# Kernel optimization log

Measured on AMD Instinct MI355X. Metric: run time of the kernel, lower is better.

The kernel has to match this reference:

```python
import jax, jax.numpy as jnp
import numpy as np

D_MODEL = 1440; D_INNER = 2880; D_STATE = 128; HEADDIM = 64; NHEADS = 45
D_CONV = 4; NLAYERS = 32; VOCAB = 256; CHUNK = 128
D_XBC = D_INNER + 2 * D_STATE          # 3136 conv channels
D_PROJ = 2 * D_INNER + 2 * D_STATE + NHEADS  # 6061 in_proj width
EPS = 1e-5

def silu(x):
    return x * jax.nn.sigmoid(x)

def segsum(x):
    # x: (..., T) -> (..., T, T); out[i, j] = sum_{j < k <= i} x[k], -inf above diagonal
    T = x.shape[-1]
    xe = jnp.broadcast_to(x[..., None], (*x.shape, T))
    lower = jnp.tril(jnp.ones((T, T), bool), -1)
    cs = jnp.cumsum(jnp.where(lower, xe, 0.0), axis=-2)
    return jnp.where(jnp.tril(jnp.ones((T, T), bool)), cs, -jnp.inf)

def ssd(X, A, B, C):
    # Chunked SSD (Mamba2 'ssd_minimal_discrete'). X:(b,l,h,p) pre-multiplied by dt,
    # A:(b,l,h) = dt * A_head, B/C:(b,l,n) (ngroups=1, shared across heads).
    b, l, h, p = X.shape
    n = B.shape[-1]
    c = l // CHUNK
    Xc = X.reshape(b, c, CHUNK, h, p)
    Ac = A.reshape(b, c, CHUNK, h).transpose(0, 3, 1, 2)      # (b,h,c,q)
    Bc = B.reshape(b, c, CHUNK, n)
    Cc = C.reshape(b, c, CHUNK, n)
    A_cs = jnp.cumsum(Ac, axis=-1)                            # (b,h,c,q)
    L = jnp.exp(segsum(Ac))                                   # (b,h,c,q,q) intra-chunk decay
    Y_diag = jnp.einsum('bcln,bcsn,bhcls,bcshp->bclhp', Cc, Bc, L, Xc)
    decay_states = jnp.exp(A_cs[..., -1:] - A_cs)             # (b,h,c,q)
    states = jnp.einsum('bcln,bhcl,bclhp->bchpn', Bc, decay_states, Xc)
    A_last = jnp.pad(A_cs[..., -1], ((0, 0), (0, 0), (1, 0)))  # (b,h,c+1)
    decay_chunk = jnp.exp(segsum(A_last))                     # (b,h,c+1,c+1)
    states = jnp.concatenate([jnp.zeros_like(states[:, :1]), states], axis=1)
    states = jnp.einsum('bhzc,bchpn->bzhpn', decay_chunk, states)[:, :-1]  # (b,c,h,p,n)
    Y_off = jnp.einsum('bcln,bchpn,bhcl->bclhp', Cc, states, jnp.exp(A_cs))
    return (Y_diag + Y_off).reshape(b, l, h, p)

def mamba2_block(h, p):
    Win, conv_w, conv_b, dt_bias, A_log, Dp, norm_w, Wout = p
    b, l, _ = h.shape
    zxbcdt = h @ Win                                           # (b,l,6061)
    z = zxbcdt[..., :D_INNER]
    xBC = zxbcdt[..., D_INNER:D_INNER + D_XBC]
    dt = jax.nn.softplus(zxbcdt[..., -NHEADS:] + dt_bias)      # (b,l,H)
    # causal depthwise conv over time, kernel 4
    xp = jnp.pad(xBC, ((0, 0), (D_CONV - 1, 0), (0, 0))).transpose(0, 2, 1)  # (b,C,l+3)
    xBC = jax.lax.conv_general_dilated(xp, conv_w[:, None, :], (1,), 'VALID',
            feature_group_count=D_XBC, dimension_numbers=('NCH', 'OIH', 'NCH'))
    xBC = silu(xBC.transpose(0, 2, 1) + conv_b)                # (b,l,3136)
    x = xBC[..., :D_INNER].reshape(b, l, NHEADS, HEADDIM)
    B = xBC[..., D_INNER:D_INNER + D_STATE]
    C = xBC[..., D_INNER + D_STATE:]
    A = -jnp.exp(A_log)                                        # (H,)
    y = ssd(x * dt[..., None], dt * A, B, C)
    y = y + x * Dp[None, None, :, None]                        # D skip (on raw x)
    y = y.reshape(b, l, D_INNER) * silu(z)                     # gate, then RMSNormGated
    y = y * jax.lax.rsqrt(jnp.mean(y * y, -1, keepdims=True) + EPS) * norm_w
    return y @ Wout

def setup_inputs() -> dict:
    key = jax.random.key(0)
    ks = jax.random.split(key, 8)
    b, l = 2, 2048
    def nrm(k, shape, s=0.02):
        return jax.random.normal(k, shape, jnp.float32) * s
    tokens = jax.random.randint(ks[0], (b, l), 0, VOCAB)
    embed = nrm(ks[1], (VOCAB, D_MODEL))
    Win = nrm(ks[2], (NLAYERS, D_MODEL, D_PROJ))
    conv_w = nrm(ks[3], (NLAYERS, D_XBC, D_CONV), 0.2)
    conv_b = jnp.zeros((NLAYERS, D_XBC), jnp.float32)
    dtv = jnp.exp(jax.random.uniform(ks[4], (NLAYERS, NHEADS)) * (np.log(0.1) - np.log(1e-3)) + np.log(1e-3))
    dt_bias = dtv + jnp.log(-jnp.expm1(-dtv))                  # inverse softplus
    A_log = jnp.log(jax.random.uniform(ks[5], (NLAYERS, NHEADS), minval=1.0, maxval=16.0))
    Dp = jnp.ones((NLAYERS, NHEADS), jnp.float32)
    norm_w = jnp.ones((NLAYERS, D_INNER), jnp.float32)
    Wout = nrm(ks[6], (NLAYERS, D_INNER, D_MODEL))
    final_norm_w = jnp.ones((D_MODEL,), jnp.float32)
    return {'tokens': tokens, 'embed': embed, 'Win': Win, 'conv_w': conv_w,
            'conv_b': conv_b, 'dt_bias': dt_bias, 'A_log': A_log, 'Dp': Dp,
            'norm_w': norm_w, 'Wout': Wout, 'final_norm_w': final_norm_w}

def reference(tokens, embed, Win, conv_w, conv_b, dt_bias, A_log, Dp, norm_w, Wout, final_norm_w):
    h = embed[tokens]                                          # (b,l,d)
    layer_params = (Win, conv_w, conv_b, dt_bias, A_log, Dp, norm_w, Wout)
    def step(carry, p):
        return carry + mamba2_block(carry, p), None
    h, _ = jax.lax.scan(jax.checkpoint(step), h, layer_params)
    h = h * jax.lax.rsqrt(jnp.mean(h * h, -1, keepdims=True) + EPS) * final_norm_w
    return h @ embed.T                                         # tied head -> (b,l,256)
```

## Files before the change

### kernel.cpp

```cpp
#include <hip/hip_runtime.h>
#include <hip/hip_bf16.h>
#include <math.h>

#define NLAYERS 32
#define DM 1440
#define DI 2880
#define DSTATE 128
#define HD 64
#define NH 45
#define VOCABSZ 256
#define CHUNK 128
#define DXBC 3136
#define DPROJ 6061
#define BB 2
#define LL 2048
#define ROWS (BB*LL)
#define NCH (LL/CHUNK)
#define ZXS 6144
#define STR 136
#define STR2 68

typedef __attribute__((ext_vector_type(8))) short bf16x8;
typedef __attribute__((ext_vector_type(4))) float f32x4;
typedef unsigned short us;

__device__ __forceinline__ float sigmoidf_(float x){ return 1.0f/(1.0f+__expf(-x)); }
__device__ __forceinline__ us f2b(float f){
  unsigned int u = __float_as_uint(f);
  return (us)((u + 0x7FFFu + ((u>>16)&1u)) >> 16);
}
__device__ __forceinline__ float b2f(us s){
  return __uint_as_float(((unsigned int)s)<<16);
}
__device__ __forceinline__ void split2(float v, us* ph, us* pl){
  us h = f2b(v);
  *ph = h;
  *pl = f2b(v - b2f(h));
}
__device__ __forceinline__ void gl2lds16(const us* g, us* l){
  __builtin_amdgcn_global_load_lds((const __attribute__((address_space(1))) unsigned int*)g,
                                   (__attribute__((address_space(3))) unsigned int*)l, 16, 0, 0);
}
#define MFMA(a,b,c) __builtin_amdgcn_mfma_f32_16x16x32_bf16(a,b,c,0,0,0)

__global__ void k_embed(const int* __restrict__ tok, const float* __restrict__ emb, float* __restrict__ h){
  int idx = blockIdx.x*256 + threadIdx.x;
  if (idx >= ROWS*DM) return;
  int row = idx / DM, d = idx - row*DM;
  h[idx] = emb[tok[row]*DM + d];
}

__global__ void k_split_rows(const float* __restrict__ src, us* __restrict__ dh,
                             us* __restrict__ dl, int ncols){
  size_t e = ((size_t)blockIdx.x*256 + threadIdx.x)*8;
  const float* s = src + e;
  bf16x8 oh, ol;
  #pragma unroll
  for (int j=0;j<8;j++){
    float v = s[j];
    us hh = f2b(v);
    ((us*)&oh)[j] = hh;
    ((us*)&ol)[j] = f2b(v - b2f(hh));
  }
  *(bf16x8*)(dh + e) = oh;
  *(bf16x8*)(dl + e) = ol;
}

__global__ void k_transcast_sp(const float* __restrict__ W, us* __restrict__ WTh,
                               us* __restrict__ WTl, int K, int N){
  __shared__ float t[32][65];
  int tid = threadIdx.x;
  int n0 = blockIdx.x*64, k0 = blockIdx.y*32;
  #pragma unroll
  for (int i=0;i<8;i++){
    int e = i*256 + tid;
    int r = e >> 6, cc = e & 63;
    int n = n0 + cc;
    t[r][cc] = (n < N) ? W[(size_t)(k0+r)*N + n] : 0.f;
  }
  __syncthreads();
  int nrow = tid >> 2, kseg = (tid & 3)*8;
  bf16x8 oh, ol;
  #pragma unroll
  for (int j=0;j<8;j++){
    float v = t[kseg+j][nrow];
    us hh = f2b(v);
    ((us*)&oh)[j] = hh;
    ((us*)&ol)[j] = f2b(v - b2f(hh));
  }
  *(bf16x8*)(WTh + (size_t)(n0+nrow)*K + k0 + kseg) = oh;
  *(bf16x8*)(WTl + (size_t)(n0+nrow)*K + k0 + kseg) = ol;
}

template<bool ACC, bool SPL>
__global__ __launch_bounds__(256) void k_gemm_sp(const us* __restrict__ Ah, const us* __restrict__ Al,
      const us* __restrict__ Bh, const us* __restrict__ Bl, float* __restrict__ C,
      int K, int ldc, int N, int nbx, us* __restrict__ Oh, us* __restrict__ Ol){
  __shared__ __align__(16) us sAh[4096], sAl[4096], sBh[4096], sBl[4096];
  int nwg = gridDim.x;
  int q = nwg >> 3;
  int bid = blockIdx.x;
  int wg = (bid & 7)*q + (bid >> 3);
  int grp = wg / (4*nbx);
  int rem = wg - grp*4*nbx;
  int by = grp*4 + (rem & 3);
  int bx = rem >> 2;
  int m0 = by*128, n0 = bx*128;
  int tid = threadIdx.x;
  int lane = tid & 63, wid = tid >> 6;
  int wr = wid >> 1, wc = wid & 1;
  int r4 = lane >> 2, c4 = (lane & 3)*8;
  int fr = lane & 15, fk = (lane >> 4)*8;
  f32x4 acc[4][4];
  #pragma unroll
  for (int i=0;i<4;i++)
    #pragma unroll
    for (int j=0;j<4;j++) acc[i][j] = (f32x4){0.f,0.f,0.f,0.f};
  for (int kt = 0; kt < K; kt += 32){
    __syncthreads();
    size_t ra0 = (size_t)(m0 + wid*16     + r4)*K + kt + c4;
    size_t ra1 = (size_t)(m0 + (wid+4)*16 + r4)*K + kt + c4;
    size_t rb0 = (size_t)(n0 + wid*16     + r4)*K + kt + c4;
    size_t rb1 = (size_t)(n0 + (wid+4)*16 + r4)*K + kt + c4;
    gl2lds16(Ah + ra0, sAh + wid*512);
    gl2lds16(Ah + ra1, sAh + (wid+4)*512);
    gl2lds16(Al + ra0, sAl + wid*512);
    gl2lds16(Al + ra1, sAl + (wid+4)*512);
    gl2lds16(Bh + rb0, sBh + wid*512);
    gl2lds16(Bh + rb1, sBh + (wid+4)*512);
    gl2lds16(Bl + rb0, sBl + wid*512);
    gl2lds16(Bl + rb1, sBl + (wid+4)*512);
    __syncthreads();
    bf16x8 ah[4], al[4], bh[4], bl[4];
    #pragma unroll
    for (int i=0;i<4;i++){
      int ro = (wr*64 + i*16 + fr)*32 + fk;
      int co = (wc*64 + i*16 + fr)*32 + fk;
      ah[i] = *(const bf16x8*)(sAh + ro);
      al[i] = *(const bf16x8*)(sAl + ro);
      bh[i] = *(const bf16x8*)(sBh + co);
      bl[i] = *(const bf16x8*)(sBl + co);
    }
    #pragma unroll
    for (int i=0;i<4;i++)
      #pragma unroll
      for (int j=0;j<4;j++){
        acc[i][j] = MFMA(ah[i], bh[j], acc[i][j]);
        acc[i][j] = MFMA(ah[i], bl[j], acc[i][j]);
        acc[i][j] = MFMA(al[i], bh[j], acc[i][j]);
      }
  }
  int orow = (lane>>4)*4, ocol = lane & 15;
  #pragma unroll
  for (int i=0;i<4;i++)
    #pragma unroll
    for (int j=0;j<4;j++)
      #pragma unroll
      for (int r=0;r<4;r++){
        int col = n0 + wc*64 + j*16 + ocol;
        if (col < N){
          size_t off = (size_t)(m0 + wr*64 + i*16 + orow + r)*ldc + col;
          float v = acc[i][j][r] + (ACC ? C[off] : 0.f);
          C[off] = v;
          if (SPL) split2(v, &Oh[off], &Ol[off]);
        }
      }
}

__global__ __launch_bounds__(256) void k_conv2(const float* __restrict__ zx, const float* __restrict__ cw,
                        const float* __restrict__ cb, us* __restrict__ xbh, us* __restrict__ xbl,
                        const float* __restrict__ dtb_in, float* __restrict__ dtb){
  int ch = blockIdx.x*256 + threadIdx.x;
  int l0 = blockIdx.y * 16;
  int b = blockIdx.z;
  if (ch < DXBC){
    float w0 = cw[ch*4+0], w1 = cw[ch*4+1], w2 = cw[ch*4+2], w3 = cw[ch*4+3];
    float bias = cb[ch];
    float x0=0.f, x1=0.f, x2=0.f;
    if (l0-3 >= 0) x0 = zx[(size_t)(b*LL + l0-3)*ZXS + DI + ch];
    if (l0-2 >= 0) x1 = zx[(size_t)(b*LL + l0-2)*ZXS + DI + ch];
    if (l0-1 >= 0) x2 = zx[(size_t)(b*LL + l0-1)*ZXS + DI + ch];
    #pragma unroll 4
    for (int l = l0; l < l0+16; ++l){
      float x3 = zx[(size_t)(b*LL + l)*ZXS + DI + ch];
      float s = bias + w0*x0 + w1*x1 + w2*x2 + w3*x3;
      float v = s * sigmoidf_(s);
      size_t off = (size_t)(b*LL + l)*DXBC + ch;
      split2(v, &xbh[off], &xbl[off]);
      x0 = x1; x1 = x2; x2 = x3;
    }
  } else if (ch < DXBC + NH){
    int hh = ch - DXBC;
    float bias = dtb_in[hh];
    #pragma unroll 4
    for (int l = l0; l < l0+16; ++l){
      size_t row = (size_t)(b*LL + l);
      float v = zx[row*ZXS + (DI+DXBC) + hh] + bias;
      dtb[row*NH + hh] = (v > 20.f) ? v : log1pf(__expf(v));
    }
  }
}

__global__ __launch_bounds__(256) void k_sraw(const us* __restrict__ xbh, const us* __restrict__ xbl,
                                              float* __restrict__ Sraw){
  __shared__ __align__(16) us sCh[128*STR], sCl[128*STR], sB2h[128*STR], sB2l[128*STR];
  int tid = threadIdx.x;
  int c = blockIdx.x, b = blockIdx.y;
  int t0 = b*LL + c*CHUNK;
  #pragma unroll
  for (int i=0;i<8;i++){
    int e = i*256 + tid;
    int l = e >> 4, seg = (e & 15)*8;
    size_t oc = (size_t)(t0+l)*DXBC + DI + DSTATE + seg;
    size_t ob = (size_t)(t0+l)*DXBC + DI + seg;
    *(bf16x8*)(sCh + l*STR + seg) = *(const bf16x8*)(xbh + oc);
    *(bf16x8*)(sCl + l*STR + seg) = *(const bf16x8*)(xbl + oc);
    *(bf16x8*)(sB2h + l*STR + seg) = *(const bf16x8*)(xbh + ob);
    *(bf16x8*)(sB2l + l*STR + seg) = *(const bf16x8*)(xbl + ob);
  }
  __syncthreads();
  int lane = tid & 63, wid = tid >> 6;
  int wbase = wid*32;
  int fr = lane & 15, fk = (lane>>4)*8;
  int orow = (lane>>4)*4;
  f32x4 accS[2][8];
  #pragma unroll
  for (int m=0;m<2;m++)
    #pragma unroll
    for (int j=0;j<8;j++) accS[m][j] = (f32x4){0.f,0.f,0.f,0.f};
  #pragma unroll
  for (int ks=0; ks<4; ++ks){
    int ko = ks*32 + fk;
    bf16x8 a0h = *(const bf16x8*)(sCh + (wbase+fr)*STR + ko);
    bf16x8 a0l = *(const bf16x8*)(sCl + (wbase+fr)*STR + ko);
    bf16x8 a1h = *(const bf16x8*)(sCh + (wbase+16+fr)*STR + ko);
    bf16x8 a1l = *(const bf16x8*)(sCl + (wbase+16+fr)*STR + ko);
    #pragma unroll
    for (int j=0;j<8;j++){
      bf16x8 bh = *(const bf16x8*)(sB2h + (j*16+fr)*STR + ko);
      bf16x8 bl = *(const bf16x8*)(sB2l + (j*16+fr)*STR + ko);
      accS[0][j] = MFMA(a0h, bh, accS[0][j]);
      accS[0][j] = MFMA(a0h, bl, accS[0][j]);
      accS[0][j] = MFMA(a0l, bh, accS[0][j]);
      accS[1][j] = MFMA(a1h, bh, accS[1][j]);
      accS[1][j] = MFMA(a1h, bl, accS[1][j]);
      accS[1][j] = MFMA(a1l, bh, accS[1][j]);
    }
  }
  size_t sbase = ((size_t)(b*NCH + c))*16384;
  #pragma unroll
  for (int m=0;m<2;m++)
    #pragma unroll
    for (int j=0;j<8;j++)
      #pragma unroll
      for (int r=0;r<4;r++){
        int l = wbase + m*16 + orow + r;
        int s = j*16 + fr;
        Sraw[sbase + l*128 + s] = accS[m][j][r];
      }
}

__global__ __launch_bounds__(256) void k_ssd_state_sp(const us* __restrict__ xbh, const us* __restrict__ xbl,
    const float* __restrict__ dtb, const float* __restrict__ Alog,
    float* __restrict__ acs, us* __restrict__ cst_h, us* __restrict__ cst_l){
  __shared__ __align__(16) us sBTh[64*STR], sBTl[64*STR];
  __shared__ __align__(16) us sXTh[64*STR], sXTl[64*STR];
  __shared__ float sAcs[128];
  __shared__ float sDt[128];
  int tid = threadIdx.x;
  int hh = blockIdx.x, c = blockIdx.y, b = blockIdx.z;
  int t0 = b*LL + c*CHUNK;
  float A_h = -__expf(Alog[hh]);
  if (tid < 128){
    float d = dtb[(size_t)(t0+tid)*NH + hh];
    sDt[tid] = d;
    sAcs[tid] = d * A_h;
  }
  __syncthreads();
  if (tid < 64){
    float v = sAcs[tid], w = sAcs[64+tid];
    #pragma unroll
    for (int off=1; off<64; off<<=1){
      float tv = __shfl_up(v, off, 64);
      float tw = __shfl_up(w, off, 64);
      if (tid >= off){ v += tv; w += tw; }
    }
    float tot = __shfl(v, 63, 64);
    sAcs[tid] = v;
    sAcs[64+tid] = w + tot;
  }
  __syncthreads();
  if (tid < 128) acs[(size_t)(t0+tid)*NH + hh] = sAcs[tid];
  float alast = sAcs[127];
  #pragma unroll 8
  for (int i=0;i<32;i++){
    int e = i*256 + tid;
    int l = e >> 6, p = e & 63;
    size_t off = (size_t)(t0+l)*DXBC + hh*HD + p;
    float v = (b2f(xbh[off]) + b2f(xbl[off])) * sDt[l] * __expf(alast - sAcs[l]);
    split2(v, &sXTh[p*STR+l], &sXTl[p*STR+l]);
  }
  int lane = tid & 63, wid = tid >> 6;
  int fr = lane & 15, fk = (lane>>4)*8;
  f32x4 acc[8];
  #pragma unroll
  for (int j=0;j<8;j++) acc[j] = (f32x4){0.f,0.f,0.f,0.f};
  #pragma unroll
  for (int nh=0; nh<2; ++nh){
    __syncthreads();
    #pragma unroll 8
    for (int i=0;i<32;i++){
      int e = i*256 + tid;
      int l = e >> 6, n = e & 63;
      size_t off = (size_t)(t0+l)*DXBC + DI + nh*64 + n;
      sBTh[n*STR+l] = xbh[off];
      sBTl[n*STR+l] = xbl[off];
    }
    __syncthreads();
    #pragma unroll
    for (int ks=0; ks<4; ks++){
      bf16x8 ah = *(const bf16x8*)(sXTh + (wid*16 + fr)*STR + ks*32 + fk);
      bf16x8 al = *(const bf16x8*)(sXTl + (wid*16 + fr)*STR + ks*32 + fk);
      #pragma unroll
      for (int j=0;j<4;j++){
        bf16x8 bh = *(const bf16x8*)(sBTh + (j*16 + fr)*STR + ks*32 + fk);
        bf16x8 bl = *(const bf16x8*)(sBTl + (j*16 + fr)*STR + ks*32 + fk);
        acc[nh*4+j] = MFMA(ah, bh, acc[nh*4+j]);
        acc[nh*4+j] = MFMA(ah, bl, acc[nh*4+j]);
        acc[nh*4+j] = MFMA(al, bh, acc[nh*4+j]);
      }
    }
  }
  size_t cbase = (((size_t)(b*NCH + c)*NH) + hh)*8192;
  int orow = (lane>>4)*4;
  #pragma unroll
  for (int jj=0;jj<8;jj++)
    #pragma unroll
    for (int r=0;r<4;r++){
      int p = wid*16 + orow + r;
      int n = (jj>>2)*64 + (jj&3)*16 + fr;
      split2(acc[jj][r], &cst_h[cbase + p*128 + n], &cst_l[cbase + p*128 + n]);
    }
}

__global__ __launch_bounds__(256) void k_ssd_scan2(const float* __restrict__ acs,
      us* __restrict__ cst_h, us* __restrict__ cst_l){
  int tid = threadIdx.x;
  int hh = blockIdx.x, b = blockIdx.y, z = blockIdx.z;
  int base_e = z*1024;
  float P[4];
  #pragma unroll
  for (int i=0;i<4;i++) P[i] = 0.f;
  for (int c=0;c<NCH;c++){
    size_t base = (((size_t)(b*NCH + c)*NH) + hh)*8192 + base_e;
    float dec = __expf(acs[(size_t)(b*LL + c*CHUNK + CHUNK-1)*NH + hh]);
    #pragma unroll
    for (int i=0;i<4;i++){
      size_t e = base + i*256 + tid;
      float tmp = b2f(cst_h[e]) + b2f(cst_l[e]);
      split2(P[i], &cst_h[e], &cst_l[e]);
      P[i] = dec*P[i] + tmp;
    }
  }
}

__global__ __launch_bounds__(512) void k_ssd_y_sp(const us* __restrict__ xbh, const us* __restrict__ xbl,
    const float* __restrict__ dtb, const float* __restrict__ acs,
    const us* __restrict__ cst_h, const us* __restrict__ cst_l,
    const float* __restrict__ Sraw, float* __restrict__ Yf){
  __shared__ __align__(16) us sXh[64*STR], sXl[64*STR];
  __shared__ float sAcs[128];
  __shared__ float sDt[128];
  int tid = threadIdx.x;
  int hh = blockIdx.x, c = blockIdx.y, b = blockIdx.z;
  int t0 = b*LL + c*CHUNK;
  if (tid < 128){
    sAcs[tid] = acs[(size_t)(t0+tid)*NH + hh];
    sDt[tid]  = dtb[(size_t)(t0+tid)*NH + hh];
  }
  #pragma unroll 8
  for (int i=0;i<16;i++){
    int e = i*512 + tid;
    int s = e >> 6, p = e & 63;
    size_t off = (size_t)(t0+s)*DXBC + hh*HD + p;
    sXh[p*STR + s] = xbh[off];
    sXl[p*STR + s] = xbl[off];
  }
  __syncthreads();
  int lane = tid & 63, wid = tid >> 6;
  int wbase = wid*16;
  int fr = lane & 15, fk = (lane>>4)*8;
  int orow = (lane>>4)*4;
  int l = wbase + fr;
  float acs_l = sAcs[l];
  size_t cbase = (((size_t)(b*NCH + c)*NH) + hh)*8192;
  size_t sbase = ((size_t)(b*NCH + c))*16384;
  size_t crow  = (size_t)(t0+l)*DXBC + DI + DSTATE;

  f32x4 accU[4], accD[4];
  #pragma unroll
  for (int j=0;j<4;j++){
    accU[j] = (f32x4){0.f,0.f,0.f,0.f};
    accD[j] = (f32x4){0.f,0.f,0.f,0.f};
  }
  #pragma unroll
  for (int kk=0; kk<4; ++kk){
    int ko = kk*32 + fk;
    bf16x8 ch8 = *(const bf16x8*)(xbh + crow + ko);
    bf16x8 cl8 = *(const bf16x8*)(xbl + crow + ko);
    #pragma unroll
    for (int j=0;j<4;j++){
      int prow = j*16 + fr;
      bf16x8 ph = *(const bf16x8*)(cst_h + cbase + prow*128 + ko);
      bf16x8 pl = *(const bf16x8*)(cst_l + cbase + prow*128 + ko);
      accU[j] = MFMA(ch8, ph, accU[j]);
      accU[j] = MFMA(ch8, pl, accU[j]);
      accU[j] = MFMA(cl8, ph, accU[j]);
    }
  }
  #pragma unroll
  for (int kk=0; kk<4; ++kk){
    int sc = kk*32 + fk;
    const float* rp = Sraw + sbase + (size_t)l*128 + sc;
    bf16x8 ah, al;
    #pragma unroll
    for (int jj=0;jj<8;jj++){
      int s = sc + jj;
      float v = (s <= l) ? rp[jj]*__expf(acs_l - sAcs[s])*sDt[s] : 0.f;
      us h2 = f2b(v);
      ((us*)&ah)[jj] = h2;
      ((us*)&al)[jj] = f2b(v - b2f(h2));
    }
    #pragma unroll
    for (int j=0;j<4;j++){
      bf16x8 xh = *(const bf16x8*)(sXh + (j*16+fr)*STR + sc);
      bf16x8 xl = *(const bf16x8*)(sXl + (j*16+fr)*STR + sc);
      accD[j] = MFMA(ah, xh, accD[j]);
      accD[j] = MFMA(ah, xl, accD[j]);
      accD[j] = MFMA(al, xh, accD[j]);
    }
  }
  #pragma unroll
  for (int r=0;r<4;r++){
    int lo = wbase + orow + r;
    float ea = __expf(sAcs[lo]);
    #pragma unroll
    for (int j=0;j<4;j++)
      Yf[(size_t)(t0+lo)*DI + hh*HD + j*16 + fr] = accD[j][r] + ea*accU[j][r];
  }
}

__global__ __launch_bounds__(256) void k_gatenorm(const float* __restrict__ Yf,
                           const us* __restrict__ xbh, const us* __restrict__ xbl,
                           const float* __restrict__ zx, const float* __restrict__ Dp_l,
                           const float* __restrict__ nw, us* __restrict__ yh, us* __restrict__ yl){
  __shared__ float red[4];
  __shared__ float stot;
  int row = blockIdx.x;
  int tid = threadIdx.x;
  float yv_[12];
  float ss = 0.f;
  #pragma unroll
  for (int i=0;i<12;i++){
    int d = tid + i*256;
    if (d < DI){
      size_t xo = (size_t)row*DXBC + d;
      float xv = b2f(xbh[xo]) + b2f(xbl[xo]);
      float yv = Yf[(size_t)row*DI + d] + xv * Dp_l[d >> 6];
      float zv = zx[(size_t)row*ZXS + d];
      yv *= zv * sigmoidf_(zv);
      yv_[i] = yv;
      ss += yv*yv;
    } else yv_[i] = 0.f;
  }
  #pragma unroll
  for (int off=32; off>0; off>>=1) ss += __shfl_down(ss, off, 64);
  int lane = tid & 63, wid = tid >> 6;
  if (lane == 0) red[wid] = ss;
  __syncthreads();
  if (tid == 0) stot = red[0]+red[1]+red[2]+red[3];
  __syncthreads();
  float rs = rsqrtf(stot / (float)DI + 1e-5f);
  #pragma unroll
  for (int i=0;i<12;i++){
    int d = tid + i*256;
    if (d < DI){
      float v = yv_[i] * rs * nw[d];
      split2(v, &yh[(size_t)row*DI + d], &yl[(size_t)row*DI + d]);
    }
  }
}

__global__ __launch_bounds__(256) void k_finalnorm(const float* __restrict__ h, const float* __restrict__ fnw,
                            us* __restrict__ oh, us* __restrict__ ol){
  __shared__ float red[4];
  __shared__ float stot;
  int row = blockIdx.x;
  int tid = threadIdx.x;
  float v_[6];
  float ss = 0.f;
  #pragma unroll
  for (int i=0;i<6;i++){
    int d = tid + i*256;
    if (d < DM){ v_[i] = h[(size_t)row*DM + d]; ss += v_[i]*v_[i]; }
    else v_[i] = 0.f;
  }
  #pragma unroll
  for (int off=32; off>0; off>>=1) ss += __shfl_down(ss, off, 64);
  int lane = tid & 63, wid = tid >> 6;
  if (lane == 0) red[wid] = ss;
  __syncthreads();
  if (tid == 0) stot = red[0]+red[1]+red[2]+red[3];
  __syncthreads();
  float rs = rsqrtf(stot / (float)DM + 1e-5f);
  #pragma unroll
  for (int i=0;i<6;i++){
    int d = tid + i*256;
    if (d < DM){
      float v = v_[i] * rs * fnw[d];
      split2(v, &oh[(size_t)row*DM + d], &ol[(size_t)row*DM + d]);
    }
  }
}

extern "C" void kernel_launch(void* const* d_in, const int* in_sizes, int n_in,
                              void* d_out, int out_size, void* d_ws, size_t ws_size,
                              hipStream_t stream){
  const int*   tok   = (const int*)d_in[0];
  const float* emb   = (const float*)d_in[1];
  const float* Win   = (const float*)d_in[2];
  const float* convw = (const float*)d_in[3];
  const float* convb = (const float*)d_in[4];
  const float* dtbias= (const float*)d_in[5];
  const float* Alog  = (const float*)d_in[6];
  const float* Dp    = (const float*)d_in[7];
  const float* normw = (const float*)d_in[8];
  const float* Wout  = (const float*)d_in[9];
  const float* fnw   = (const float*)d_in[10];

  float* ws = (float*)d_ws;
  float* h    = ws;
  float* zx   = ws + 5898240;
  us*    xbh  = (us*)(ws + 31064064);
  us*    xbl  = (us*)(ws + 37486592);
  us*    hp_h = (us*)(ws + 31064064);
  us*    hp_l = (us*)(ws + 34013184);
  float* dtb  = ws + 43909120;
  float* acs  = ws + 44093440;
  float* Yf   = ws + 44277760;
  us* wbuf_h  = (us*)(ws + 44277760);
  us* wbuf_l  = (us*)(ws + 48701440);
  us* cst_h   = (us*)(ws + 56074240);
  us* cst_l   = (us*)(ws + 61972480);
  us* ab_h    = (us*)(ws + 56074240);
  us* ab_l    = (us*)(ws + 61972480);
  float* Sraw = ws + 67870720;

  k_embed<<<(ROWS*DM+255)/256, 256, 0, stream>>>(tok, emb, h);
  k_split_rows<<<2880, 256, 0, stream>>>(h, hp_h, hp_l, DM);
  for (int lyr=0; lyr<NLAYERS; ++lyr){
    k_transcast_sp<<<dim3(ZXS/64, DM/32), 256, 0, stream>>>(Win + (size_t)lyr*DM*DPROJ, wbuf_h, wbuf_l, DM, DPROJ);
    k_gemm_sp<false,false><<<(ZXS/128)*(ROWS/128), 256, 0, stream>>>(hp_h, hp_l, wbuf_h, wbuf_l, zx, DM, ZXS, ZXS, ZXS/128, nullptr, nullptr);
    k_conv2<<<dim3(13, 128, BB), 256, 0, stream>>>(
        zx, convw + (size_t)lyr*DXBC*4, convb + (size_t)lyr*DXBC, xbh, xbl,
        dtbias + lyr*NH, dtb);
    k_sraw<<<dim3(NCH, BB), 256, 0, stream>>>(xbh, xbl, Sraw);
    k_ssd_state_sp<<<dim3(NH, NCH, BB), 256, 0, stream>>>(xbh, xbl, dtb, Alog + lyr*NH, acs, cst_h, cst_l);
    k_ssd_scan2<<<dim3(NH, BB, 8), 256, 0, stream>>>(acs, cst_h, cst_l);
    k_ssd_y_sp<<<dim3(NH, NCH, BB), 512, 0, stream>>>(xbh, xbl, dtb, acs, cst_h, cst_l, Sraw, Yf);
    k_gatenorm<<<ROWS, 256, 0, stream>>>(Yf, xbh, xbl, zx, Dp + lyr*NH, normw + (size_t)lyr*DI, ab_h, ab_l);
    k_transcast_sp<<<dim3(1536/64, DI/32), 256, 0, stream>>>(Wout + (size_t)lyr*DI*DM, wbuf_h, wbuf_l, DI, DM);
    k_gemm_sp<true,true><<<(1536/128)*(ROWS/128), 256, 0, stream>>>(ab_h, ab_l, wbuf_h, wbuf_l, h, DI, DM, DM, 1536/128, hp_h, hp_l);
  }
  k_finalnorm<<<ROWS, 256, 0, stream>>>(h, fnw, ab_h, ab_l);
  k_split_rows<<<180, 256, 0, stream>>>(emb, wbuf_h, wbuf_l, DM);
  k_gemm_sp<false,false><<<(VOCABSZ/128)*(ROWS/128), 256, 0, stream>>>(ab_h, ab_l, wbuf_h, wbuf_l, (float*)d_out, DM, VOCABSZ, VOCABSZ, VOCABSZ/128, nullptr, nullptr);
}
```

Measured before the change: 19.63 ms.

## Precompute transposed B per chunk once in sraw; read it directly in state kernel

```diff
diff --git a/kernel.cpp b/kernel.cpp
--- a/kernel.cpp
+++ b/kernel.cpp
@@ -202,7 +202,8 @@
 }
 
 __global__ __launch_bounds__(256) void k_sraw(const us* __restrict__ xbh, const us* __restrict__ xbl,
-                                              float* __restrict__ Sraw){
+                                              float* __restrict__ Sraw,
+                                              us* __restrict__ BTh, us* __restrict__ BTl){
   __shared__ __align__(16) us sCh[128*STR], sCl[128*STR], sB2h[128*STR], sB2l[128*STR];
   int tid = threadIdx.x;
   int c = blockIdx.x, b = blockIdx.y;
@@ -219,6 +220,14 @@
     *(bf16x8*)(sB2l + l*STR + seg) = *(const bf16x8*)(xbl + ob);
   }
   __syncthreads();
+  size_t btb = ((size_t)(b*NCH + c))*16384;
+  #pragma unroll
+  for (int i=0;i<64;i++){
+    int e = i*256 + tid;
+    int n = e >> 7, l = e & 127;
+    BTh[btb + n*128 + l] = sB2h[l*STR + n];
+    BTl[btb + n*128 + l] = sB2l[l*STR + n];
+  }
   int lane = tid & 63, wid = tid >> 6;
   int wbase = wid*32;
   int fr = lane & 15, fk = (lane>>4)*8;
@@ -260,10 +269,10 @@
       }
 }
 
-__global__ __launch_bounds__(256) void k_ssd_state_sp(const us* __restrict__ xbh, const us* __restrict__ xbl,
+__global__ __launch_bounds__(512) void k_ssd_state_sp(const us* __restrict__ xbh, const us* __restrict__ xbl,
     const float* __restrict__ dtb, const float* __restrict__ Alog,
+    const us* __restrict__ BTh, const us* __restrict__ BTl,
     float* __restrict__ acs, us* __restrict__ cst_h, us* __restrict__ cst_l){
-  __shared__ __align__(16) us sBTh[64*STR], sBTl[64*STR];
   __shared__ __align__(16) us sXTh[64*STR], sXTl[64*STR];
   __shared__ float sAcs[128];
   __shared__ float sDt[128];
@@ -293,53 +302,46 @@
   if (tid < 128) acs[(size_t)(t0+tid)*NH + hh] = sAcs[tid];
   float alast = sAcs[127];
   #pragma unroll 8
-  for (int i=0;i<32;i++){
-    int e = i*256 + tid;
+  for (int i=0;i<16;i++){
+    int e = i*512 + tid;
     int l = e >> 6, p = e & 63;
     size_t off = (size_t)(t0+l)*DXBC + hh*HD + p;
     float v = (b2f(xbh[off]) + b2f(xbl[off])) * sDt[l] * __expf(alast - sAcs[l]);
     split2(v, &sXTh[p*STR+l], &sXTl[p*STR+l]);
   }
+  __syncthreads();
   int lane = tid & 63, wid = tid >> 6;
   int fr = lane & 15, fk = (lane>>4)*8;
-  f32x4 acc[8];
-  #pragma unroll
-  for (int j=0;j<8;j++) acc[j] = (f32x4){0.f,0.f,0.f,0.f};
-  #pragma unroll
-  for (int nh=0; nh<2; ++nh){
-    __syncthreads();
-    #pragma unroll 8
-    for (int i=0;i<32;i++){
-      int e = i*256 + tid;
-      int l = e >> 6, n = e & 63;
-      size_t off = (size_t)(t0+l)*DXBC + DI + nh*64 + n;
-      sBTh[n*STR+l] = xbh[off];
-      sBTl[n*STR+l] = xbl[off];
-    }
-    __syncthreads();
-    #pragma unroll
-    for (int ks=0; ks<4; ks++){
-      bf16x8 ah = *(const bf16x8*)(sXTh + (wid*16 + fr)*STR + ks*32 + fk);
-      bf16x8 al = *(const bf16x8*)(sXTl + (wid*16 + fr)*STR + ks*32 + fk);
-      #pragma unroll
-      for (int j=0;j<4;j++){
-        bf16x8 bh = *(const bf16x8*)(sBTh + (j*16 + fr)*STR + ks*32 + fk);
-        bf16x8 bl = *(const bf16x8*)(sBTl + (j*16 + fr)*STR + ks*32 + fk);
-        acc[nh*4+j] = MFMA(ah, bh, acc[nh*4+j]);
-        acc[nh*4+j] = MFMA(ah, bl, acc[nh*4+j]);
-        acc[nh*4+j] = MFMA(al, bh, acc[nh*4+j]);
-      }
+  int pr = (wid & 3)*16;
+  int nb = (wid >> 2)*64;
+  size_t btb = ((size_t)(b*NCH + c))*16384;
+  f32x4 acc[4];
+  #pragma unroll
+  for (int j=0;j<4;j++) acc[j] = (f32x4){0.f,0.f,0.f,0.f};
+  #pragma unroll
+  for (int ks=0; ks<4; ks++){
+    int ko = ks*32 + fk;
+    bf16x8 ah = *(const bf16x8*)(sXTh + (pr + fr)*STR + ko);
+    bf16x8 al = *(const bf16x8*)(sXTl + (pr + fr)*STR + ko);
+    #pragma unroll
+    for (int j=0;j<4;j++){
+      int nrow = nb + j*16 + fr;
+      bf16x8 bh = *(const bf16x8*)(BTh + btb + nrow*128 + ko);
+      bf16x8 bl = *(const bf16x8*)(BTl + btb + nrow*128 + ko);
+      acc[j] = MFMA(ah, bh, acc[j]);
+      acc[j] = MFMA(ah, bl, acc[j]);
+      acc[j] = MFMA(al, bh, acc[j]);
     }
   }
   size_t cbase = (((size_t)(b*NCH + c)*NH) + hh)*8192;
   int orow = (lane>>4)*4;
   #pragma unroll
-  for (int jj=0;jj<8;jj++)
+  for (int j=0;j<4;j++)
     #pragma unroll
     for (int r=0;r<4;r++){
-      int p = wid*16 + orow + r;
-      int n = (jj>>2)*64 + (jj&3)*16 + fr;
-      split2(acc[jj][r], &cst_h[cbase + p*128 + n], &cst_l[cbase + p*128 + n]);
+      int p = pr + orow + r;
+      int n = nb + j*16 + fr;
+      split2(acc[j][r], &cst_h[cbase + p*128 + n], &cst_l[cbase + p*128 + n]);
     }
 }
 
@@ -555,6 +557,8 @@
   us* ab_h    = (us*)(ws + 56074240);
   us* ab_l    = (us*)(ws + 61972480);
   float* Sraw = ws + 67870720;
+  us*    BTh  = (us*)(ws + 68395008);
+  us*    BTl  = (us*)(ws + 68657152);
 
   k_embed<<<(ROWS*DM+255)/256, 256, 0, stream>>>(tok, emb, h);
   k_split_rows<<<2880, 256, 0, stream>>>(h, hp_h, hp_l, DM);
@@ -564,8 +568,8 @@
     k_conv2<<<dim3(13, 128, BB), 256, 0, stream>>>(
         zx, convw + (size_t)lyr*DXBC*4, convb + (size_t)lyr*DXBC, xbh, xbl,
         dtbias + lyr*NH, dtb);
-    k_sraw<<<dim3(NCH, BB), 256, 0, stream>>>(xbh, xbl, Sraw);
-    k_ssd_state_sp<<<dim3(NH, NCH, BB), 256, 0, stream>>>(xbh, xbl, dtb, Alog + lyr*NH, acs, cst_h, cst_l);
+    k_sraw<<<dim3(NCH, BB), 256, 0, stream>>>(xbh, xbl, Sraw, BTh, BTl);
+    k_ssd_state_sp<<<dim3(NH, NCH, BB), 512, 0, stream>>>(xbh, xbl, dtb, Alog + lyr*NH, BTh, BTl, acs, cst_h, cst_l);
     k_ssd_scan2<<<dim3(NH, BB, 8), 256, 0, stream>>>(acs, cst_h, cst_l);
     k_ssd_y_sp<<<dim3(NH, NCH, BB), 512, 0, stream>>>(xbh, xbl, dtb, acs, cst_h, cst_l, Sraw, Yf);
     k_gatenorm<<<ROWS, 256, 0, stream>>>(Yf, xbh, xbl, zx, Dp + lyr*NH, normw + (size_t)lyr*DI, ab_h, ab_l);
```

Result: slower. 20.15 ms (+2.6%).

## Fuse weight transpose-casts into GEMM launches and swizzle LDS transpose stores

Applied to the files above, without the earlier changes.

```diff
diff --git a/kernel.cpp b/kernel.cpp
--- a/kernel.cpp
+++ b/kernel.cpp
@@ -18,7 +18,6 @@
 #define NCH (LL/CHUNK)
 #define ZXS 6144
 #define STR 136
-#define STR2 68
 
 typedef __attribute__((ext_vector_type(8))) short bf16x8;
 typedef __attribute__((ext_vector_type(4))) float f32x4;
@@ -95,18 +94,46 @@
 template<bool ACC, bool SPL>
 __global__ __launch_bounds__(256) void k_gemm_sp(const us* __restrict__ Ah, const us* __restrict__ Al,
       const us* __restrict__ Bh, const us* __restrict__ Bl, float* __restrict__ C,
-      int K, int ldc, int N, int nbx, us* __restrict__ Oh, us* __restrict__ Ol){
-  __shared__ __align__(16) us sAh[4096], sAl[4096], sBh[4096], sBl[4096];
-  int nwg = gridDim.x;
-  int q = nwg >> 3;
+      int K, int ldc, int N, int nbx, us* __restrict__ Oh, us* __restrict__ Ol,
+      int ngemm, const float* __restrict__ tcW, us* __restrict__ tcH, us* __restrict__ tcL,
+      int tcK, int tcN, int tcNBX){
+  __shared__ __align__(16) us smem[16384];
   int bid = blockIdx.x;
+  int tid = threadIdx.x;
+  if (bid >= ngemm){
+    int t = bid - ngemm;
+    int n0 = (t % tcNBX)*64, k0 = (t / tcNBX)*32;
+    float* tt = (float*)smem;
+    #pragma unroll
+    for (int i=0;i<8;i++){
+      int e = i*256 + tid;
+      int r = e >> 6, cc = e & 63;
+      int n = n0 + cc;
+      tt[r*65+cc] = (n < tcN) ? tcW[(size_t)(k0+r)*tcN + n] : 0.f;
+    }
+    __syncthreads();
+    int nrow = tid >> 2, kseg = (tid & 3)*8;
+    bf16x8 oh, ol;
+    #pragma unroll
+    for (int j=0;j<8;j++){
+      float v = tt[(kseg+j)*65 + nrow];
+      us hh = f2b(v);
+      ((us*)&oh)[j] = hh;
+      ((us*)&ol)[j] = f2b(v - b2f(hh));
+    }
+    *(bf16x8*)(tcH + (size_t)(n0+nrow)*tcK + k0 + kseg) = oh;
+    *(bf16x8*)(tcL + (size_t)(n0+nrow)*tcK + k0 + kseg) = ol;
+    return;
+  }
+  us* sAh = smem;        us* sAl = smem + 4096;
+  us* sBh = smem + 8192; us* sBl = smem + 12288;
+  int q = ngemm >> 3;
   int wg = (bid & 7)*q + (bid >> 3);
   int grp = wg / (4*nbx);
   int rem = wg - grp*4*nbx;
   int by = grp*4 + (rem & 3);
   int bx = rem >> 2;
   int m0 = by*128, n0 = bx*128;
-  int tid = threadIdx.x;
   int lane = tid & 63, wid = tid >> 6;
   int wr = wid >> 1, wc = wid & 1;
   int r4 = lane >> 2, c4 = (lane & 3)*8;
@@ -294,8 +321,9 @@
   float alast = sAcs[127];
   #pragma unroll 8
   for (int i=0;i<32;i++){
-    int e = i*256 + tid;
-    int l = e >> 6, p = e & 63;
+    int idx = i*256 + tid;
+    int j = idx & 7, g = (idx>>3) & 7, pm = (idx>>6) & 7, lm = idx>>9;
+    int p = pm*8 + j, l = lm*8 + g;
     size_t off = (size_t)(t0+l)*DXBC + hh*HD + p;
     float v = (b2f(xbh[off]) + b2f(xbl[off])) * sDt[l] * __expf(alast - sAcs[l]);
     split2(v, &sXTh[p*STR+l], &sXTl[p*STR+l]);
@@ -310,8 +338,9 @@
     __syncthreads();
     #pragma unroll 8
     for (int i=0;i<32;i++){
-      int e = i*256 + tid;
-      int l = e >> 6, n = e & 63;
+      int idx = i*256 + tid;
+      int j = idx & 7, g = (idx>>3) & 7, nm = (idx>>6) & 7, lm = idx>>9;
+      int n = nm*8 + j, l = lm*8 + g;
       size_t off = (size_t)(t0+l)*DXBC + DI + nh*64 + n;
       sBTh[n*STR+l] = xbh[off];
       sBTl[n*STR+l] = xbl[off];
@@ -380,8 +409,9 @@
   }
   #pragma unroll 8
   for (int i=0;i<16;i++){
-    int e = i*512 + tid;
-    int s = e >> 6, p = e & 63;
+    int idx = i*512 + tid;
+    int j = idx & 7, g = (idx>>3) & 7, pm = (idx>>6) & 7, lm = idx>>9;
+    int p = pm*8 + j, s = lm*8 + g;
     size_t off = (size_t)(t0+s)*DXBC + hh*HD + p;
     sXh[p*STR + s] = xbh[off];
     sXl[p*STR + s] = xbl[off];
@@ -548,19 +578,23 @@
   float* dtb  = ws + 43909120;
   float* acs  = ws + 44093440;
   float* Yf   = ws + 44277760;
-  us* wbuf_h  = (us*)(ws + 44277760);
-  us* wbuf_l  = (us*)(ws + 48701440);
   us* cst_h   = (us*)(ws + 56074240);
   us* cst_l   = (us*)(ws + 61972480);
   us* ab_h    = (us*)(ws + 56074240);
   us* ab_l    = (us*)(ws + 61972480);
   float* Sraw = ws + 67870720;
+  us* winh    = (us*)(ws + 68395008);
+  us* winl    = (us*)(ws + 72818688);
+  us* wouth   = (us*)(ws + 77242368);
+  us* woutl   = (us*)(ws + 79454208);
 
   k_embed<<<(ROWS*DM+255)/256, 256, 0, stream>>>(tok, emb, h);
   k_split_rows<<<2880, 256, 0, stream>>>(h, hp_h, hp_l, DM);
+  k_transcast_sp<<<dim3(ZXS/64, DM/32), 256, 0, stream>>>(Win, winh, winl, DM, DPROJ);
   for (int lyr=0; lyr<NLAYERS; ++lyr){
-    k_transcast_sp<<<dim3(ZXS/64, DM/32), 256, 0, stream>>>(Win + (size_t)lyr*DM*DPROJ, wbuf_h, wbuf_l, DM, DPROJ);
-    k_gemm_sp<false,false><<<(ZXS/128)*(ROWS/128), 256, 0, stream>>>(hp_h, hp_l, wbuf_h, wbuf_l, zx, DM, ZXS, ZXS, ZXS/128, nullptr, nullptr);
+    k_gemm_sp<false,false><<<1536 + 2160, 256, 0, stream>>>(
+        hp_h, hp_l, winh, winl, zx, DM, ZXS, ZXS, ZXS/128, nullptr, nullptr,
+        1536, Wout + (size_t)lyr*DI*DM, wouth, woutl, DI, DM, 24);
     k_conv2<<<dim3(13, 128, BB), 256, 0, stream>>>(
         zx, convw + (size_t)lyr*DXBC*4, convb + (size_t)lyr*DXBC, xbh, xbl,
         dtbias + lyr*NH, dtb);
@@ -569,10 +603,19 @@
     k_ssd_scan2<<<dim3(NH, BB, 8), 256, 0, stream>>>(acs, cst_h, cst_l);
     k_ssd_y_sp<<<dim3(NH, NCH, BB), 512, 0, stream>>>(xbh, xbl, dtb, acs, cst_h, cst_l, Sraw, Yf);
     k_gatenorm<<<ROWS, 256, 0, stream>>>(Yf, xbh, xbl, zx, Dp + lyr*NH, normw + (size_t)lyr*DI, ab_h, ab_l);
-    k_transcast_sp<<<dim3(1536/64, DI/32), 256, 0, stream>>>(Wout + (size_t)lyr*DI*DM, wbuf_h, wbuf_l, DI, DM);
-    k_gemm_sp<true,true><<<(1536/128)*(ROWS/128), 256, 0, stream>>>(ab_h, ab_l, wbuf_h, wbuf_l, h, DI, DM, DM, 1536/128, hp_h, hp_l);
+    if (lyr+1 < NLAYERS){
+      k_gemm_sp<true,true><<<384 + 4320, 256, 0, stream>>>(
+          ab_h, ab_l, wouth, woutl, h, DI, DM, DM, 1536/128, hp_h, hp_l,
+          384, Win + (size_t)(lyr+1)*DM*DPROJ, winh, winl, DM, DPROJ, 96);
+    } else {
+      k_gemm_sp<true,true><<<384, 256, 0, stream>>>(
+          ab_h, ab_l, wouth, woutl, h, DI, DM, DM, 1536/128, hp_h, hp_l,
+          384, nullptr, nullptr, nullptr, 0, 0, 1);
+    }
   }
   k_finalnorm<<<ROWS, 256, 0, stream>>>(h, fnw, ab_h, ab_l);
-  k_split_rows<<<180, 256, 0, stream>>>(emb, wbuf_h, wbuf_l, DM);
-  k_gemm_sp<false,false><<<(VOCABSZ/128)*(ROWS/128), 256, 0, stream>>>(ab_h, ab_l, wbuf_h, wbuf_l, (float*)d_out, DM, VOCABSZ, VOCABSZ, VOCABSZ/128, nullptr, nullptr);
-}
+  k_split_rows<<<180, 256, 0, stream>>>(emb, wouth, woutl, DM);
+  k_gemm_sp<false,false><<<(VOCABSZ/128)*(ROWS/128), 256, 0, stream>>>(
+      ab_h, ab_l, wouth, woutl, (float*)d_out, DM, VOCABSZ, VOCABSZ, VOCABSZ/128, nullptr, nullptr,
+      (VOCABSZ/128)*(ROWS/128), nullptr, nullptr, nullptr, 0, 0, 1);
+}
```

New measurement: 18.98 ms. -3.3%, faster.
